# Kernel tuning notes

Hardware: AMD Instinct MI355X
Metric: run time of the kernel (lower is better)

## Reference

```python
import jax, jax.numpy as jnp
import numpy as np
from jax import lax

# ---- config mirroring the torch module (eval path) ----
IMG_H, IMG_W = 1280, 1280   # stride 8 * 160 feature map
FEAT = 160
STRIDE = 8
SIZES = (32.0, 64.0, 128.0)
RATIOS = (0.5, 1.0, 2.0)
BATCH = 4
MAX_DETS = 1000             # eval: keep[:min(1000, len(keep))]
IOU_THRESH = 0.5
DW_CLAMP = 4.0


def _make_anchors():
    # anchor grid [FEAT*FEAT*A, 4] in xyxy, same for every image
    ctr = (np.arange(FEAT, dtype=np.float32) + 0.5) * STRIDE
    cy, cx = np.meshgrid(ctr, ctr, indexing='ij')          # [F,F]
    whs = []
    for s in SIZES:
        for r in RATIOS:
            whs.append((s * np.sqrt(r), s / np.sqrt(r)))
    whs = np.asarray(whs, dtype=np.float32)                 # [A,2]
    cx = cx[..., None]; cy = cy[..., None]                  # [F,F,1]
    w = whs[:, 0]; h = whs[:, 1]                            # [A]
    boxes = np.stack([cx - 0.5 * w, cy - 0.5 * h,
                      cx + 0.5 * w, cy + 0.5 * h], axis=-1)  # [F,F,A,4]
    return boxes.reshape(-1, 4)                              # [N,4]


def setup_inputs() -> dict:
    key = jax.random.key(0)
    k1, k2 = jax.random.split(key)
    N = FEAT * FEAT * len(SIZES) * len(RATIOS)
    anchors = jnp.asarray(np.broadcast_to(_make_anchors(), (BATCH, N, 4)).copy())
    objectness = jax.random.normal(k1, (BATCH, N), dtype=jnp.float32)
    deltas = jax.random.normal(k2, (BATCH, N, 4), dtype=jnp.float32) * 0.2
    return {"objectness": objectness, "deltas": deltas, "anchors": anchors}


def _decode_boxes(deltas, anchors):
    # faithful to CascadeRCNN.decode_boxes (with dw/dh clamp(max=4))
    w = anchors[:, 2] - anchors[:, 0]
    h = anchors[:, 3] - anchors[:, 1]
    cx = anchors[:, 0] + 0.5 * w
    cy = anchors[:, 1] + 0.5 * h
    px = deltas[:, 0] * w + cx
    py = deltas[:, 1] * h + cy
    pw = jnp.exp(jnp.minimum(deltas[:, 2], DW_CLAMP)) * w
    ph = jnp.exp(jnp.minimum(deltas[:, 3], DW_CLAMP)) * h
    return jnp.stack([px - 0.5 * pw, py - 0.5 * ph,
                      px + 0.5 * pw, py + 0.5 * ph], axis=-1)


def _nms(boxes, scores, valid):
    # greedy NMS: fixed MAX_DETS iterations, fixed shapes (jit-safe).
    areas = jnp.maximum(boxes[:, 2] - boxes[:, 0], 0.0) * \
            jnp.maximum(boxes[:, 3] - boxes[:, 1], 0.0)
    ms0 = jnp.where(valid, scores, -1.0)   # sigmoid scores are > 0

    def step(ms, _):
        idx = jnp.argmax(ms)
        s = ms[idx]
        b = boxes[idx]
        ix1 = jnp.maximum(b[0], boxes[:, 0])
        iy1 = jnp.maximum(b[1], boxes[:, 1])
        ix2 = jnp.minimum(b[2], boxes[:, 2])
        iy2 = jnp.minimum(b[3], boxes[:, 3])
        inter = jnp.maximum(ix2 - ix1, 0.0) * jnp.maximum(iy2 - iy1, 0.0)
        iou = inter / (areas[idx] + areas - inter + 1e-9)
        sel_ok = s > 0.0
        ms = jnp.where((iou > IOU_THRESH) & sel_ok, -1.0, ms)
        ms = ms.at[idx].set(-1.0)   # always retire the picked slot
        return ms, (idx, sel_ok)

    _, (idxs, sel_valid) = lax.scan(step, ms0, None, length=MAX_DETS)
    return idxs, sel_valid


def _per_image(objectness, deltas, anchors):
    scores = jax.nn.sigmoid(objectness)
    props = _decode_boxes(deltas, anchors)
    # clip_boxes_to_image
    x = jnp.clip(props[:, 0::2], 0.0, float(IMG_W))
    y = jnp.clip(props[:, 1::2], 0.0, float(IMG_H))
    props = jnp.stack([x[:, 0], y[:, 0], x[:, 1], y[:, 1]], axis=-1)
    # remove_small_boxes(min_size=1) as a mask (fixed shapes)
    valid = ((props[:, 2] - props[:, 0]) >= 1.0) & ((props[:, 3] - props[:, 1]) >= 1.0)
    idxs, sel_valid = _nms(props, scores, valid)
    m = sel_valid.astype(props.dtype)
    out_boxes = props[idxs] * m[:, None]       # [MAX_DETS,4], zero-padded
    out_scores = scores[idxs] * m              # [MAX_DETS]
    return out_boxes, out_scores, sel_valid


def reference(objectness, deltas, anchors):
    # objectness [B,N], deltas [B,N,4], anchors [B,N,4]
    boxes, scores, valid = jax.vmap(_per_image)(objectness, deltas, anchors)
    return boxes, scores, valid
```

## Files before the change

kernel.cpp:

```cpp
#include <hip/hip_runtime.h>
#include <stdint.h>

typedef unsigned long long u64;
typedef unsigned int u32;

#define BATCH 4
#define NANCH 230400
#define NBLK  900
#define SELCAP 8192
#define CPROC 4096
#define NJC   8
#define MAXD 1000
#define IMGW 1280.0f
#define IMGH 1280.0f

#define DSC_TH 0x40970A3Cu

#define BLKCNT_OFF 0
#define BLKVAL_OFF (BLKCNT_OFF + BATCH*NBLK*4)
#define BLKOFF_OFF (BLKVAL_OFF + BATCH*NBLK*4)
#define SELCNT_OFF (BLKOFF_OFF + BATCH*NBLK*4)
#define TOTVAL_OFF (SELCNT_OFF + BATCH*4)
#define SCORE_OFF  65536
#define DESC_OFF   (SCORE_OFF + BATCH*NANCH*4)
#define BOX_OFF    (DESC_OFF + BATCH*NANCH*4)
#define SELKEY_OFF (BOX_OFF + (size_t)BATCH*NANCH*16)
#define SBOX_OFF   (SELKEY_OFF + (size_t)BATCH*SELCAP*8)
#define SSCORE_OFF (SBOX_OFF + (size_t)BATCH*SELCAP*16)
#define SAREA_OFF  (SSCORE_OFF + (size_t)BATCH*SELCAP*4)
#define PART_OFF   (SAREA_OFF + (size_t)BATCH*SELCAP*4)
#define MASK_OFF   (PART_OFF + (size_t)BATCH*SELCAP*NJC*4)

__global__ void decode_kernel(const float* __restrict__ obj,
                              const float4* __restrict__ deltas,
                              const float4* __restrict__ anchors,
                              float* __restrict__ score, u32* __restrict__ desc,
                              float4* __restrict__ boxes,
                              u32* __restrict__ blockcnt, u32* __restrict__ blockval) {
    int gid = blockIdx.x * blockDim.x + threadIdx.x;
    int img = blockIdx.x / NBLK;
    int ai = gid - img * NANCH;
    float4 a = anchors[ai];
    float4 d = deltas[gid];
    float o = obj[gid];
    float w = __fsub_rn(a.z, a.x), h = __fsub_rn(a.w, a.y);
    float cx = __fadd_rn(a.x, __fmul_rn(0.5f, w));
    float cy = __fadd_rn(a.y, __fmul_rn(0.5f, h));
    float px = __fadd_rn(__fmul_rn(d.x, w), cx);
    float py = __fadd_rn(__fmul_rn(d.y, h), cy);
    float pw = __fmul_rn(expf(fminf(d.z, 4.0f)), w);
    float ph = __fmul_rn(expf(fminf(d.w, 4.0f)), h);
    float x1 = __fsub_rn(px, __fmul_rn(0.5f, pw));
    float y1 = __fsub_rn(py, __fmul_rn(0.5f, ph));
    float x2 = __fadd_rn(px, __fmul_rn(0.5f, pw));
    float y2 = __fadd_rn(py, __fmul_rn(0.5f, ph));
    x1 = fminf(fmaxf(x1, 0.0f), IMGW); x2 = fminf(fmaxf(x2, 0.0f), IMGW);
    y1 = fminf(fmaxf(y1, 0.0f), IMGH); y2 = fminf(fmaxf(y2, 0.0f), IMGH);
    bool valid = (__fsub_rn(x2, x1) >= 1.0f) && (__fsub_rn(y2, y1) >= 1.0f);
    float s = __fdiv_rn(1.0f, __fadd_rn(1.0f, expf(-o)));
    boxes[gid] = make_float4(x1, y1, x2, y2);
    score[gid] = s;
    u32 dsc = valid ? (0x7FFFFFFFu - __float_as_uint(s)) : 0xFFFFFFFFu;
    desc[gid] = dsc;
    bool pass = dsc <= DSC_TH;
    u64 bp = __ballot(pass);
    u64 bv = __ballot(valid);
    __shared__ u32 wcnt[4], wval[4];
    int wid = threadIdx.x >> 6;
    if ((threadIdx.x & 63) == 0) { wcnt[wid] = (u32)__popcll(bp); wval[wid] = (u32)__popcll(bv); }
    __syncthreads();
    if (threadIdx.x == 0) {
        blockcnt[blockIdx.x] = wcnt[0] + wcnt[1] + wcnt[2] + wcnt[3];
        blockval[blockIdx.x] = wval[0] + wval[1] + wval[2] + wval[3];
    }
}

__global__ void scan_kernel(const u32* __restrict__ blockcnt, const u32* __restrict__ blockval,
                            u32* __restrict__ blockoff, u32* __restrict__ selcnt,
                            u32* __restrict__ totval) {
    int img = blockIdx.x, t = threadIdx.x;
    int lane = t & 63, wv = t >> 6;
    const u32* BC = blockcnt + img * NBLK;
    u32* BO = blockoff + img * NBLK;
    __shared__ u32 wsum[4], wsumv[4];
    int i0 = t * 4;
    u32 c[4], s = 0;
    for (int k = 0; k < 4; k++) { int i = i0 + k; c[k] = (i < NBLK) ? BC[i] : 0u; s += c[k]; }
    u32 v = 0;
    for (int k = 0; k < 4; k++) { int i = i0 + k; v += (i < NBLK) ? blockval[img * NBLK + i] : 0u; }
    u32 x = s, xv = v;
    #pragma unroll
    for (int off = 1; off < 64; off <<= 1) {
        u32 y = __shfl_up(x, off);
        u32 yv = __shfl_up(xv, off);
        if (lane >= off) { x += y; xv += yv; }
    }
    if (lane == 63) { wsum[wv] = x; wsumv[wv] = xv; }
    __syncthreads();
    u32 wbase = 0;
    for (int w = 0; w < wv; w++) wbase += wsum[w];
    u32 run = wbase + (x - s);
    for (int k = 0; k < 4; k++) { int i = i0 + k; if (i < NBLK) BO[i] = run; run += c[k]; }
    if (t == 0) {
        selcnt[img] = wsum[0] + wsum[1] + wsum[2] + wsum[3];
        totval[img] = wsumv[0] + wsumv[1] + wsumv[2] + wsumv[3];
    }
}

__global__ void scatter_kernel(const u32* __restrict__ desc, const u32* __restrict__ blockoff,
                               u64* __restrict__ selkey) {
    int blk = blockIdx.x, tid = threadIdx.x;
    int gid = blk * 256 + tid;
    int img = blk / NBLK;
    u32 d = desc[gid];
    bool pass = d <= DSC_TH;
    u64 bal = __ballot(pass);
    int lane = tid & 63, wid = tid >> 6;
    __shared__ u32 woff[4];
    if (lane == 0) woff[wid] = (u32)__popcll(bal);
    __syncthreads();
    u32 wbase = 0;
    for (int w = 0; w < wid; w++) wbase += woff[w];
    if (pass) {
        u32 pos = blockoff[blk] + wbase + (u32)__popcll(bal & ((1ull << lane) - 1ull));
        if (pos < SELCAP)
            selkey[(size_t)img * SELCAP + pos] = ((u64)d << 32) | (u32)(gid - img * NANCH);
    }
}

__global__ void rankpart_kernel(const u64* __restrict__ selkey, const u32* __restrict__ selcnt,
                                u32* __restrict__ partial) {
    int img = blockIdx.z;
    int C = min((int)selcnt[img], SELCAP);
    if ((int)(blockIdx.x * 256) >= C) return;
    int tid = threadIdx.x;
    int i = blockIdx.x * 256 + tid;
    int jc = blockIdx.y;
    int chunk = (C + NJC - 1) / NJC;
    int j0 = jc * chunk, j1 = min(j0 + chunk, C);
    const u64* K = selkey + (size_t)img * SELCAP;
    __shared__ u64 tile[1024];
    bool act = i < C;
    u64 my = act ? K[i] : ~0ull;
    u32 r = 0;
    for (int t0 = j0; t0 < j1; t0 += 1024) {
        int cnt = min(1024, j1 - t0);
        __syncthreads();
        for (int j = tid; j < cnt; j += 256) tile[j] = K[t0 + j];
        __syncthreads();
        int j = 0;
        for (; j + 8 <= cnt; j += 8) {
            u64 a0 = tile[j], a1 = tile[j+1], a2 = tile[j+2], a3 = tile[j+3];
            u64 a4 = tile[j+4], a5 = tile[j+5], a6 = tile[j+6], a7 = tile[j+7];
            r += (a0 < my) + (a1 < my) + (a2 < my) + (a3 < my)
               + (a4 < my) + (a5 < my) + (a6 < my) + (a7 < my);
        }
        for (; j < cnt; j++) r += (tile[j] < my) ? 1u : 0u;
    }
    if (act) partial[((size_t)img * SELCAP + i) * NJC + jc] = r;
}

__global__ void rankgather_kernel(const u64* __restrict__ selkey, const u32* __restrict__ selcnt,
                                  const u32* __restrict__ partial,
                                  const float4* __restrict__ boxes, const float* __restrict__ score,
                                  float4* __restrict__ sbox, float* __restrict__ sscore,
                                  float* __restrict__ sarea) {
    int img = blockIdx.y;
    int C = min((int)selcnt[img], SELCAP);
    if ((int)(blockIdx.x * 256) >= C) return;
    int i = blockIdx.x * 256 + threadIdx.x;
    if (i >= C) return;
    const u32* P = partial + ((size_t)img * SELCAP + i) * NJC;
    u32 rank = 0;
    #pragma unroll
    for (int k = 0; k < NJC; k++) rank += P[k];
    u64 my = selkey[(size_t)img * SELCAP + i];
    int ai = (int)(my & 0xFFFFFFFFu);
    int g = img * NANCH + ai;
    float4 bx = boxes[g];
    size_t o = (size_t)img * SELCAP + rank;
    sbox[o] = bx;
    sscore[o] = score[g];
    sarea[o] = __fmul_rn(fmaxf(__fsub_rn(bx.z, bx.x), 0.0f),
                         fmaxf(__fsub_rn(bx.w, bx.y), 0.0f));
}

__global__ void mask_kernel(const float4* __restrict__ sbox, const float* __restrict__ sarea,
                            const u32* __restrict__ selcnt, u64* __restrict__ mask) {
    int img = blockIdx.z;
    int C = min((int)selcnt[img], SELCAP);
    int Ce = min(C, CPROC);
    int bx = blockIdx.x;
    if (bx * 256 >= Ce) return;
    int jt = blockIdx.y;
    int jtmax = (Ce + 63) >> 6;
    if (jt >= jtmax || jt < bx * 4) return;
    int i = bx * 256 + threadIdx.x;
    const float4* SB = sbox + (size_t)img * SELCAP;
    const float* SA = sarea + (size_t)img * SELCAP;
    __shared__ float jx1[64], jy1[64], jx2[64], jy2[64], jar[64];
    int jbase = jt << 6;
    int jcnt = min(64, Ce - jbase);
    bool act = (i < Ce) && (jt >= ((i >> 7) << 1));
    float4 bi = make_float4(0, 0, 0, 0);
    float ai_ = 0.0f;
    if (act) { bi = SB[i]; ai_ = SA[i]; }
    if (threadIdx.x < 64) {
        int l = threadIdx.x;
        if (l < jcnt) {
            float4 b = SB[jbase + l];
            jx1[l] = b.x; jy1[l] = b.y; jx2[l] = b.z; jy2[l] = b.w;
            jar[l] = SA[jbase + l];
        } else {
            jx1[l] = 0; jy1[l] = 0; jx2[l] = 0; jy2[l] = 0; jar[l] = 0;
        }
    }
    __syncthreads();
    if (!act) return;
    u64 bits = 0;
    if (jcnt == 64) {
        #pragma unroll 8
        for (int jl = 0; jl < 64; jl++) {
            float ix1 = fmaxf(bi.x, jx1[jl]);
            float iy1 = fmaxf(bi.y, jy1[jl]);
            float ix2 = fminf(bi.z, jx2[jl]);
            float iy2 = fminf(bi.w, jy2[jl]);
            float inter = __fmul_rn(fmaxf(__fsub_rn(ix2, ix1), 0.0f),
                                    fmaxf(__fsub_rn(iy2, iy1), 0.0f));
            float den = __fadd_rn(__fsub_rn(__fadd_rn(ai_, jar[jl]), inter), 1e-9f);
            if (__fdiv_rn(inter, den) > 0.5f) bits |= (1ull << jl);
        }
    } else {
        for (int jl = 0; jl < jcnt; jl++) {
            float ix1 = fmaxf(bi.x, jx1[jl]);
            float iy1 = fmaxf(bi.y, jy1[jl]);
            float ix2 = fminf(bi.z, jx2[jl]);
            float iy2 = fminf(bi.w, jy2[jl]);
            float inter = __fmul_rn(fmaxf(__fsub_rn(ix2, ix1), 0.0f),
                                    fmaxf(__fsub_rn(iy2, iy1), 0.0f));
            float den = __fadd_rn(__fsub_rn(__fadd_rn(ai_, jar[jl]), inter), 1e-9f);
            if (__fdiv_rn(inter, den) > 0.5f) bits |= (1ull << jl);
        }
    }
    mask[((size_t)img * CPROC + (size_t)i) * 64 + jt] = bits;
}

#define BAR_LDS() do { \
    asm volatile("s_waitcnt lgkmcnt(0)" ::: "memory"); \
    __builtin_amdgcn_s_barrier(); \
    asm volatile("" ::: "memory"); \
} while (0)

__global__ __launch_bounds__(256, 1)
void sweep_kernel(const float4* __restrict__ sbox, const float* __restrict__ sscore,
                  const float* __restrict__ sarea, const u32* __restrict__ selcnt,
                  const u32* __restrict__ totval, const u64* __restrict__ mask,
                  const u64* __restrict__ selkey, const u32* __restrict__ descarr,
                  const float4* __restrict__ boxes, const float* __restrict__ scorearr,
                  float* __restrict__ out) {
    int img = blockIdx.x;
    int tid = threadIdx.x, lane = tid & 63, wv = tid >> 6;
    int C = min((int)selcnt[img], SELCAP);
    int Ce = min(C, CPROC);
    const float4* SB = sbox + (size_t)img * SELCAP;
    const float* SS = sscore + (size_t)img * SELCAP;
    const float* SA = sarea + (size_t)img * SELCAP;
    const u64* M = mask + (size_t)img * CPROC * 64;
    const u64* K = selkey + (size_t)img * SELCAP;
    __shared__ float ax1[MAXD], ay1[MAXD], ax2[MAXD], ay2[MAXD], aar[MAXD];
    __shared__ u64 lds_sup4[4][64];
    __shared__ u64 red64[4];
    __shared__ int redi[4];
    float* ob = out + (size_t)img * MAXD * 4;
    float* os = out + (size_t)BATCH * MAXD * 4 + (size_t)img * MAXD;
    float* ov = out + (size_t)BATCH * MAXD * 5 + (size_t)img * MAXD;
    lds_sup4[wv][lane] = 0;
    int nblk2 = (Ce + 127) >> 7;
    u64 low = (1ull << lane) - 1ull;
    u64 tL0 = 0, tH0 = 0, tH1 = 0;
    float4 bcur = make_float4(0.0f, 0.0f, 0.0f, 0.0f);
    float scur = 0.0f, acur = 0.0f;
    if (nblk2 > 0) {
        int bc_lo = min(64, Ce);
        int bh = Ce - 64; int bc_hi = bh < 0 ? 0 : min(64, bh);
        if (lane < bc_lo) tL0 = M[(size_t)lane * 64 + 0];
        if (lane < bc_hi) {
            tH0 = M[(size_t)(64 + lane) * 64 + 0];
            tH1 = M[(size_t)(64 + lane) * 64 + 1];
        }
        if (wv == 0 && lane < bc_lo) { bcur = SB[lane]; scur = SS[lane]; acur = SA[lane]; }
        if (wv == 1 && lane < bc_hi) { bcur = SB[64 + lane]; scur = SS[64 + lane]; acur = SA[64 + lane]; }
    }
    __syncthreads();
    u64 psup = 0;
    int acc = 0;
    for (int kb = 0; kb < nblk2 && acc < MAXD; kb++) {
        int base = kb << 7;
        int bc_lo = min(64, Ce - base);
        int bh = Ce - base - 64; int bc_hi = bh < 0 ? 0 : min(64, bh);
        int bcount = bc_lo + bc_hi;
        int wlo = kb * 2, whi = kb * 2 + 1;
        u64 vals[32];
        #pragma unroll
        for (int k = 0; k < 32; k++) {
            int r = wv + 4 * k;
            vals[k] = (r < bcount) ? M[(size_t)(base + r) * 64 + lane] : 0ull;
        }
        bool haven = (kb + 1 < nblk2);
        int nb = base + 128;
        int nbc_lo = haven ? min(64, Ce - nb) : 0;
        int nh = haven ? (Ce - nb - 64) : 0; int nbc_hi = nh < 0 ? 0 : min(64, nh);
        u64 tL0n = 0, tH0n = 0, tH1n = 0;
        float4 bnx = make_float4(0.0f, 0.0f, 0.0f, 0.0f);
        float snx = 0.0f, anx = 0.0f;
        if (haven) {
            int wlon = wlo + 2, whin = whi + 2;
            if (lane < nbc_lo) tL0n = M[(size_t)(nb + lane) * 64 + wlon];
            if (lane < nbc_hi) {
                tH0n = M[(size_t)(nb + 64 + lane) * 64 + wlon];
                tH1n = M[(size_t)(nb + 64 + lane) * 64 + whin];
            }
            if (wv == 0 && lane < nbc_lo) { bnx = SB[nb + lane]; snx = SS[nb + lane]; anx = SA[nb + lane]; }
            if (wv == 1 && lane < nbc_hi) { bnx = SB[nb + 64 + lane]; snx = SS[nb + 64 + lane]; anx = SA[nb + 64 + lane]; }
        }
        u64 ext_lo = lds_sup4[0][wlo] | lds_sup4[1][wlo] | lds_sup4[2][wlo] | lds_sup4[3][wlo];
        u64 ext_hi = lds_sup4[0][whi] | lds_sup4[1][whi] | lds_sup4[2][whi] | lds_sup4[3][whi];
        u64 rng_lo = (bc_lo == 64) ? ~0ull : ((1ull << bc_lo) - 1ull);
        u64 rng_hi = (bc_hi == 64) ? ~0ull : ((1ull << bc_hi) - 1ull);
        u64 A0lo = ~ext_lo & rng_lo, A0hi = ~ext_hi & rng_hi;
        u64 Alo = A0lo, Ahi = A0hi;
        for (int it = 0; it < 128; it++) {
            bool supL = (tL0 & Alo & low) != 0ull;
            bool supH = ((tH0 & Alo) | (tH1 & Ahi & low)) != 0ull;
            u64 SL = __ballot(supL);
            u64 SH = __ballot(supH);
            u64 nlo = A0lo & ~SL, nhi = A0hi & ~SH;
            if (nlo == Alo && nhi == Ahi) break;
            Alo = nlo; Ahi = nhi;
        }
        int clo = __popcll(Alo), chi = __popcll(Ahi);
        int keep = MAXD - acc;
        if (clo + chi > keep) {
            if (keep <= clo) {
                Ahi = 0; chi = 0;
                while (clo > keep) { Alo &= ~(1ull << (63 - __builtin_clzll(Alo))); clo--; }
            } else {
                int kh = keep - clo;
                while (chi > kh) { Ahi &= ~(1ull << (63 - __builtin_clzll(Ahi))); chi--; }
            }
        }
        u64 nmlo = Alo, nmhi = Ahi;
        int na = clo + chi;
        if (wv == 0 && ((nmlo >> lane) & 1ull)) {
            int o = acc + __popcll(nmlo & low);
            ((float4*)ob)[o] = bcur;
            os[o] = scur; ov[o] = 1.0f;
            ax1[o] = bcur.x; ay1[o] = bcur.y; ax2[o] = bcur.z; ay2[o] = bcur.w;
            aar[o] = acur;
        }
        if (wv == 1 && ((nmhi >> lane) & 1ull)) {
            int o = acc + clo + __popcll(nmhi & low);
            ((float4*)ob)[o] = bcur;
            os[o] = scur; ov[o] = 1.0f;
            ax1[o] = bcur.x; ay1[o] = bcur.y; ax2[o] = bcur.z; ay2[o] = bcur.w;
            aar[o] = acur;
        }
        #pragma unroll
        for (int k = 0; k < 16; k++) {
            int r = wv + 4 * k;
            psup |= ((nmlo >> r) & 1ull) ? vals[k] : 0ull;
        }
        #pragma unroll
        for (int k = 16; k < 32; k++) {
            int r = wv + 4 * k - 64;
            psup |= ((nmhi >> r) & 1ull) ? vals[k] : 0ull;
        }
        lds_sup4[wv][lane] = psup;
        acc += na;
        BAR_LDS();
        tL0 = tL0n; tH0 = tH0n; tH1 = tH1n;
        bcur = bnx; scur = snx; acur = anx;
    }
    for (int i = Ce; i < C && acc < MAXD; i++) {
        float4 bx = SB[i];
        float ar = SA[i];
        bool hit = false;
        for (int k = tid; k < acc; k += 256) {
            float ix1 = fmaxf(bx.x, ax1[k]);
            float iy1 = fmaxf(bx.y, ay1[k]);
            float ix2 = fminf(bx.z, ax2[k]);
            float iy2 = fminf(bx.w, ay2[k]);
            float inter = __fmul_rn(fmaxf(__fsub_rn(ix2, ix1), 0.0f),
                                    fmaxf(__fsub_rn(iy2, iy1), 0.0f));
            float den = __fadd_rn(__fsub_rn(__fadd_rn(aar[k], ar), inter), 1e-9f);
            if (__fdiv_rn(inter, den) > 0.5f) { hit = true; break; }
        }
        u64 bal = __ballot(hit);
        if (lane == 0) redi[wv] = (bal != 0ull) ? 1 : 0;
        __syncthreads();
        bool any = (redi[0] | redi[1] | redi[2] | redi[3]) != 0;
        __syncthreads();
        if (!any) {
            if (tid == 0) {
                ob[acc * 4 + 0] = bx.x; ob[acc * 4 + 1] = bx.y;
                ob[acc * 4 + 2] = bx.z; ob[acc * 4 + 3] = bx.w;
                os[acc] = SS[i]; ov[acc] = 1.0f;
                ax1[acc] = bx.x; ay1[acc] = bx.y; ax2[acc] = bx.z; ay2[acc] = bx.w;
                aar[acc] = ar;
            }
            __syncthreads();
            acc++;
        }
    }
    u32 tv = totval[img];
    if (acc < MAXD && (u32)C < tv && (u32)C == selcnt[img]) {
        u64 lk = 0;
        for (int j = tid; j < C; j += 256) lk = max(lk, K[j]);
        for (int off = 32; off; off >>= 1) { u64 o = __shfl_down(lk, off); lk = max(lk, o); }
        if (lane == 0) red64[wv] = lk;
        __syncthreads();
        lk = max(max(red64[0], red64[1]), max(red64[2], red64[3]));
        __syncthreads();
        while (acc < MAXD) {
            u64 best = ~0ull;
            for (int j = tid; j < NANCH; j += 256) {
                u32 d = descarr[(size_t)img * NANCH + j];
                if (d != 0xFFFFFFFFu) {
                    u64 kk = ((u64)d << 32) | (u32)j;
                    if (kk > lk && kk < best) best = kk;
                }
            }
            for (int off = 32; off; off >>= 1) { u64 o = __shfl_down(best, off); best = min(best, o); }
            if (lane == 0) red64[wv] = best;
            __syncthreads();
            best = min(min(red64[0], red64[1]), min(red64[2], red64[3]));
            __syncthreads();
            if (best == ~0ull) break;
            lk = best;
            int ai = (int)(best & 0xFFFFFFFFu);
            int g = img * NANCH + ai;
            float4 bx = boxes[g];
            float ar = __fmul_rn(fmaxf(__fsub_rn(bx.z, bx.x), 0.0f),
                                 fmaxf(__fsub_rn(bx.w, bx.y), 0.0f));
            bool hit = false;
            for (int k = tid; k < acc; k += 256) {
                float ix1 = fmaxf(bx.x, ax1[k]);
                float iy1 = fmaxf(bx.y, ay1[k]);
                float ix2 = fminf(bx.z, ax2[k]);
                float iy2 = fminf(bx.w, ay2[k]);
                float inter = __fmul_rn(fmaxf(__fsub_rn(ix2, ix1), 0.0f),
                                        fmaxf(__fsub_rn(iy2, iy1), 0.0f));
                float den = __fadd_rn(__fsub_rn(__fadd_rn(aar[k], ar), inter), 1e-9f);
                if (__fdiv_rn(inter, den) > 0.5f) { hit = true; break; }
            }
            u64 bal = __ballot(hit);
            if (lane == 0) redi[wv] = (bal != 0ull) ? 1 : 0;
            __syncthreads();
            bool any = (redi[0] | redi[1] | redi[2] | redi[3]) != 0;
            __syncthreads();
            if (!any) {
                if (tid == 0) {
                    ob[acc * 4 + 0] = bx.x; ob[acc * 4 + 1] = bx.y;
                    ob[acc * 4 + 2] = bx.z; ob[acc * 4 + 3] = bx.w;
                    os[acc] = scorearr[g]; ov[acc] = 1.0f;
                    ax1[acc] = bx.x; ay1[acc] = bx.y; ax2[acc] = bx.z; ay2[acc] = bx.w;
                    aar[acc] = ar;
                }
                __syncthreads();
                acc++;
            }
        }
    }
}

extern "C" void kernel_launch(void* const* d_in, const int* in_sizes, int n_in,
                              void* d_out, int out_size, void* d_ws, size_t ws_size,
                              hipStream_t stream) {
    const float* obj = (const float*)d_in[0];
    const float4* deltas = (const float4*)d_in[1];
    const float4* anchors = (const float4*)d_in[2];
    char* ws = (char*)d_ws;
    u32* blockcnt = (u32*)(ws + BLKCNT_OFF);
    u32* blockval = (u32*)(ws + BLKVAL_OFF);
    u32* blockoff = (u32*)(ws + BLKOFF_OFF);
    u32* selcnt = (u32*)(ws + SELCNT_OFF);
    u32* totval = (u32*)(ws + TOTVAL_OFF);
    float* score = (float*)(ws + SCORE_OFF);
    u32* desc = (u32*)(ws + DESC_OFF);
    float4* boxes = (float4*)(ws + BOX_OFF);
    u64* selkey = (u64*)(ws + SELKEY_OFF);
    float4* sbox = (float4*)(ws + SBOX_OFF);
    float* sscore = (float*)(ws + SSCORE_OFF);
    float* sarea = (float*)(ws + SAREA_OFF);
    u32* partial = (u32*)(ws + PART_OFF);
    u64* mask = (u64*)(ws + MASK_OFF);
    float* out = (float*)d_out;

    size_t zfloats = (size_t)BATCH * MAXD * 6;
    if ((size_t)out_size < zfloats) zfloats = (size_t)out_size;
    hipMemsetAsync(d_out, 0, zfloats * sizeof(float), stream);

    decode_kernel<<<3600, 256, 0, stream>>>(obj, deltas, anchors, score, desc, boxes,
                                            blockcnt, blockval);
    scan_kernel<<<BATCH, 256, 0, stream>>>(blockcnt, blockval, blockoff, selcnt, totval);
    scatter_kernel<<<3600, 256, 0, stream>>>(desc, blockoff, selkey);
    rankpart_kernel<<<dim3(SELCAP / 256, NJC, BATCH), 256, 0, stream>>>(selkey, selcnt, partial);
    rankgather_kernel<<<dim3(SELCAP / 256, BATCH), 256, 0, stream>>>(selkey, selcnt, partial,
                                                                     boxes, score,
                                                                     sbox, sscore, sarea);
    mask_kernel<<<dim3(CPROC / 256, CPROC / 64, BATCH), 256, 0, stream>>>(sbox, sarea, selcnt, mask);
    sweep_kernel<<<BATCH, 256, 0, stream>>>(sbox, sscore, sarea, selcnt, totval, mask,
                                            selkey, desc, boxes, score, out);
}
```

Measured before the change: 152.5 us.

## Fuse scan into scatter, merge rank kernels, replace output memset with tail zeroing

Removes the separate scan kernel: each scatter block now computes its own prefix offset by summing preceding block counts for its image, and block 0 writes the per-image totals. The split rank-partial and rank-gather kernels are merged into one kernel that counts the full key range per element and scatters directly. The output memset is dropped and the sweep kernel zero-fills the unused tail slots instead. This removes three launches and the partial-rank round trip, at the cost of redundant prefix reads per scatter block (up to 900 loads) and less parallelism in the rank kernel.

```diff
diff --git a/kernel.cpp b/kernel.cpp
--- a/kernel.cpp
+++ b/kernel.cpp
@@ -9,7 +9,6 @@
 #define NBLK  900
 #define SELCAP 8192
 #define CPROC 4096
-#define NJC   8
 #define MAXD 1000
 #define IMGW 1280.0f
 #define IMGH 1280.0f
@@ -29,7 +28,7 @@
 #define SSCORE_OFF (SBOX_OFF + (size_t)BATCH*SELCAP*16)
 #define SAREA_OFF  (SSCORE_OFF + (size_t)BATCH*SELCAP*4)
 #define PART_OFF   (SAREA_OFF + (size_t)BATCH*SELCAP*4)
-#define MASK_OFF   (PART_OFF + (size_t)BATCH*SELCAP*NJC*4)
+#define MASK_OFF   (PART_OFF + (size_t)BATCH*SELCAP*8*4)
 
 __global__ void decode_kernel(const float* __restrict__ obj,
                               const float4* __restrict__ deltas,
@@ -75,76 +74,65 @@
     }
 }
 
-__global__ void scan_kernel(const u32* __restrict__ blockcnt, const u32* __restrict__ blockval,
-                            u32* __restrict__ blockoff, u32* __restrict__ selcnt,
-                            u32* __restrict__ totval) {
-    int img = blockIdx.x, t = threadIdx.x;
-    int lane = t & 63, wv = t >> 6;
+__global__ void scatter_kernel(const u32* __restrict__ desc,
+                               const u32* __restrict__ blockcnt,
+                               const u32* __restrict__ blockval,
+                               u64* __restrict__ selkey,
+                               u32* __restrict__ selcnt, u32* __restrict__ totval) {
+    int blk = blockIdx.x, tid = threadIdx.x;
+    int img = blk / NBLK;
+    int lblk = blk - img * NBLK;
     const u32* BC = blockcnt + img * NBLK;
-    u32* BO = blockoff + img * NBLK;
-    __shared__ u32 wsum[4], wsumv[4];
-    int i0 = t * 4;
-    u32 c[4], s = 0;
-    for (int k = 0; k < 4; k++) { int i = i0 + k; c[k] = (i < NBLK) ? BC[i] : 0u; s += c[k]; }
-    u32 v = 0;
-    for (int k = 0; k < 4; k++) { int i = i0 + k; v += (i < NBLK) ? blockval[img * NBLK + i] : 0u; }
-    u32 x = s, xv = v;
+    int lane = tid & 63, wid = tid >> 6;
+    __shared__ u32 lsum[4], s2[4], v2[4], woff[4];
+    u32 part = 0;
+    for (int i = tid; i < lblk; i += 256) part += BC[i];
     #pragma unroll
-    for (int off = 1; off < 64; off <<= 1) {
-        u32 y = __shfl_up(x, off);
-        u32 yv = __shfl_up(xv, off);
-        if (lane >= off) { x += y; xv += yv; }
-    }
-    if (lane == 63) { wsum[wv] = x; wsumv[wv] = xv; }
-    __syncthreads();
-    u32 wbase = 0;
-    for (int w = 0; w < wv; w++) wbase += wsum[w];
-    u32 run = wbase + (x - s);
-    for (int k = 0; k < 4; k++) { int i = i0 + k; if (i < NBLK) BO[i] = run; run += c[k]; }
-    if (t == 0) {
-        selcnt[img] = wsum[0] + wsum[1] + wsum[2] + wsum[3];
-        totval[img] = wsumv[0] + wsumv[1] + wsumv[2] + wsumv[3];
-    }
-}
-
-__global__ void scatter_kernel(const u32* __restrict__ desc, const u32* __restrict__ blockoff,
-                               u64* __restrict__ selkey) {
-    int blk = blockIdx.x, tid = threadIdx.x;
+    for (int off = 32; off; off >>= 1) part += __shfl_down(part, off);
+    if (lane == 0) lsum[wid] = part;
+    if (lblk == 0) {
+        u32 ts = 0, tv = 0;
+        for (int i = tid; i < NBLK; i += 256) { ts += BC[i]; tv += blockval[img * NBLK + i]; }
+        #pragma unroll
+        for (int off = 32; off; off >>= 1) { ts += __shfl_down(ts, off); tv += __shfl_down(tv, off); }
+        if (lane == 0) { s2[wid] = ts; v2[wid] = tv; }
+    }
     int gid = blk * 256 + tid;
-    int img = blk / NBLK;
     u32 d = desc[gid];
     bool pass = d <= DSC_TH;
     u64 bal = __ballot(pass);
-    int lane = tid & 63, wid = tid >> 6;
-    __shared__ u32 woff[4];
     if (lane == 0) woff[wid] = (u32)__popcll(bal);
     __syncthreads();
+    if (lblk == 0 && tid == 0) {
+        selcnt[img] = s2[0] + s2[1] + s2[2] + s2[3];
+        totval[img] = v2[0] + v2[1] + v2[2] + v2[3];
+    }
+    u32 blockoff = lsum[0] + lsum[1] + lsum[2] + lsum[3];
     u32 wbase = 0;
     for (int w = 0; w < wid; w++) wbase += woff[w];
     if (pass) {
-        u32 pos = blockoff[blk] + wbase + (u32)__popcll(bal & ((1ull << lane) - 1ull));
+        u32 pos = blockoff + wbase + (u32)__popcll(bal & ((1ull << lane) - 1ull));
         if (pos < SELCAP)
             selkey[(size_t)img * SELCAP + pos] = ((u64)d << 32) | (u32)(gid - img * NANCH);
     }
 }
 
-__global__ void rankpart_kernel(const u64* __restrict__ selkey, const u32* __restrict__ selcnt,
-                                u32* __restrict__ partial) {
-    int img = blockIdx.z;
+__global__ void rank_kernel(const u64* __restrict__ selkey, const u32* __restrict__ selcnt,
+                            const float4* __restrict__ boxes, const float* __restrict__ score,
+                            float4* __restrict__ sbox, float* __restrict__ sscore,
+                            float* __restrict__ sarea) {
+    int img = blockIdx.y;
     int C = min((int)selcnt[img], SELCAP);
     if ((int)(blockIdx.x * 256) >= C) return;
     int tid = threadIdx.x;
     int i = blockIdx.x * 256 + tid;
-    int jc = blockIdx.y;
-    int chunk = (C + NJC - 1) / NJC;
-    int j0 = jc * chunk, j1 = min(j0 + chunk, C);
     const u64* K = selkey + (size_t)img * SELCAP;
     __shared__ u64 tile[1024];
     bool act = i < C;
     u64 my = act ? K[i] : ~0ull;
     u32 r = 0;
-    for (int t0 = j0; t0 < j1; t0 += 1024) {
-        int cnt = min(1024, j1 - t0);
+    for (int t0 = 0; t0 < C; t0 += 1024) {
+        int cnt = min(1024, C - t0);
         __syncthreads();
         for (int j = tid; j < cnt; j += 256) tile[j] = K[t0 + j];
         __syncthreads();
@@ -157,28 +145,11 @@
         }
         for (; j < cnt; j++) r += (tile[j] < my) ? 1u : 0u;
     }
-    if (act) partial[((size_t)img * SELCAP + i) * NJC + jc] = r;
-}
-
-__global__ void rankgather_kernel(const u64* __restrict__ selkey, const u32* __restrict__ selcnt,
-                                  const u32* __restrict__ partial,
-                                  const float4* __restrict__ boxes, const float* __restrict__ score,
-                                  float4* __restrict__ sbox, float* __restrict__ sscore,
-                                  float* __restrict__ sarea) {
-    int img = blockIdx.y;
-    int C = min((int)selcnt[img], SELCAP);
-    if ((int)(blockIdx.x * 256) >= C) return;
-    int i = blockIdx.x * 256 + threadIdx.x;
-    if (i >= C) return;
-    const u32* P = partial + ((size_t)img * SELCAP + i) * NJC;
-    u32 rank = 0;
-    #pragma unroll
-    for (int k = 0; k < NJC; k++) rank += P[k];
-    u64 my = selkey[(size_t)img * SELCAP + i];
+    if (!act) return;
     int ai = (int)(my & 0xFFFFFFFFu);
     int g = img * NANCH + ai;
     float4 bx = boxes[g];
-    size_t o = (size_t)img * SELCAP + rank;
+    size_t o = (size_t)img * SELCAP + r;
     sbox[o] = bx;
     sscore[o] = score[g];
     sarea[o] = __fmul_rn(fmaxf(__fsub_rn(bx.z, bx.x), 0.0f),
@@ -471,6 +442,11 @@
             }
         }
     }
+    for (int o = acc + tid; o < MAXD; o += 256) {
+        ((float4*)ob)[o] = make_float4(0.0f, 0.0f, 0.0f, 0.0f);
+        os[o] = 0.0f;
+        ov[o] = 0.0f;
+    }
 }
 
 extern "C" void kernel_launch(void* const* d_in, const int* in_sizes, int n_in,
@@ -482,7 +458,6 @@
     char* ws = (char*)d_ws;
     u32* blockcnt = (u32*)(ws + BLKCNT_OFF);
     u32* blockval = (u32*)(ws + BLKVAL_OFF);
-    u32* blockoff = (u32*)(ws + BLKOFF_OFF);
     u32* selcnt = (u32*)(ws + SELCNT_OFF);
     u32* totval = (u32*)(ws + TOTVAL_OFF);
     float* score = (float*)(ws + SCORE_OFF);
@@ -492,22 +467,16 @@
     float4* sbox = (float4*)(ws + SBOX_OFF);
     float* sscore = (float*)(ws + SSCORE_OFF);
     float* sarea = (float*)(ws + SAREA_OFF);
-    u32* partial = (u32*)(ws + PART_OFF);
     u64* mask = (u64*)(ws + MASK_OFF);
     float* out = (float*)d_out;
 
-    size_t zfloats = (size_t)BATCH * MAXD * 6;
-    if ((size_t)out_size < zfloats) zfloats = (size_t)out_size;
-    hipMemsetAsync(d_out, 0, zfloats * sizeof(float), stream);
-
     decode_kernel<<<3600, 256, 0, stream>>>(obj, deltas, anchors, score, desc, boxes,
                                             blockcnt, blockval);
-    scan_kernel<<<BATCH, 256, 0, stream>>>(blockcnt, blockval, blockoff, selcnt, totval);
-    scatter_kernel<<<3600, 256, 0, stream>>>(desc, blockoff, selkey);
-    rankpart_kernel<<<dim3(SELCAP / 256, NJC, BATCH), 256, 0, stream>>>(selkey, selcnt, partial);
-    rankgather_kernel<<<dim3(SELCAP / 256, BATCH), 256, 0, stream>>>(selkey, selcnt, partial,
-                                                                     boxes, score,
-                                                                     sbox, sscore, sarea);
+    scatter_kernel<<<3600, 256, 0, stream>>>(desc, blockcnt, blockval,
+                                             selkey, selcnt, totval);
+    rank_kernel<<<dim3(SELCAP / 256, BATCH), 256, 0, stream>>>(selkey, selcnt,
+                                                               boxes, score,
+                                                               sbox, sscore, sarea);
     mask_kernel<<<dim3(CPROC / 256, CPROC / 64, BATCH), 256, 0, stream>>>(sbox, sarea, selcnt, mask);
     sweep_kernel<<<BATCH, 256, 0, stream>>>(sbox, sscore, sarea, selcnt, totval, mask,
                                             selkey, desc, boxes, score, out);
```

Measured after the change: 174.1 us. +14.2%, slower.
